# Kernel tuning notes

Hardware: AMD Instinct MI355X
Metric: run time of the kernel (lower is better)

## Reference

```python
import jax, jax.numpy as jnp
import numpy as np

N_NODES = 50000
N_EDGES = 1600000
D_IN = 128
D_HID = 128
D_OUT = 64
N_EXPERT = 16


def setup_inputs() -> dict:
    key = jax.random.key(0)
    ks = jax.random.split(key, 16)
    x = jax.random.normal(ks[0], (N_NODES, D_IN), dtype=jnp.float32)
    edge_index = jax.random.randint(ks[1], (2, N_EDGES), 0, N_NODES, dtype=jnp.int64)

    def lin(k, di, do):
        return jax.random.normal(k, (di, do), dtype=jnp.float32) / np.float32(np.sqrt(di))

    def expert_w(k, di, do):
        return jax.random.normal(k, (N_EXPERT, di, do), dtype=jnp.float32) / np.float32(np.sqrt(di))

    return {
        "x": x,
        "edge_index": edge_index,
        # layer 1 (MoE GCN conv: D_IN -> D_HID)
        "Wg1": lin(ks[2], D_IN, N_EXPERT), "bg1": jnp.zeros((N_EXPERT,), jnp.float32),
        "We1": expert_w(ks[3], D_IN, D_HID), "be1": jnp.zeros((N_EXPERT, D_HID), jnp.float32),
        "b1": jnp.zeros((D_HID,), jnp.float32),
        # layer 2 (MoE GCN conv: D_HID -> D_HID)
        "Wg2": lin(ks[4], D_HID, N_EXPERT), "bg2": jnp.zeros((N_EXPERT,), jnp.float32),
        "We2": expert_w(ks[5], D_HID, D_HID), "be2": jnp.zeros((N_EXPERT, D_HID), jnp.float32),
        "b2": jnp.zeros((D_HID,), jnp.float32),
        # layer 3 (plain GCNConv: D_HID -> D_OUT)
        "Wlast": lin(ks[6], D_HID, D_OUT), "blast": jnp.zeros((D_OUT,), jnp.float32),
    }


def _moe_linear(x, Wg, bg, We, be):
    # naive gate, top_k=1: route to argmax expert, combine weight 1.0
    scores = jax.nn.softmax(x @ Wg + bg, axis=-1)              # [N, E]
    idx = jnp.argmax(scores, axis=-1)                          # [N]
    y_all = jnp.einsum('nd,edh->neh', x, We) + be              # [N, E, H]
    onehot = jax.nn.one_hot(idx, We.shape[0], dtype=x.dtype)   # [N, E]
    y = jnp.einsum('neh,ne->nh', y_all, onehot)                # [N, H]
    return y, scores


def _scatter_add(h, edge_index, num_nodes):
    src, dst = edge_index[0], edge_index[1]
    return jax.ops.segment_sum(h[src], dst, num_segments=num_nodes)


def _moe_conv(x, edge_index, Wg, bg, We, be, bias):
    h, scores = _moe_linear(x, Wg, bg, We, be)
    out = _scatter_add(h, edge_index, x.shape[0]) + bias
    gate_std = jnp.mean(jnp.std(scores, axis=1, ddof=1))
    return out, gate_std


def reference(x, edge_index, Wg1, bg1, We1, be1, b1, Wg2, bg2, We2, be2, b2, Wlast, blast):
    # layer 1 + relu (dropout inactive in eval)
    h, g1 = _moe_conv(x, edge_index, Wg1, bg1, We1, be1, b1)
    h = jax.nn.relu(h)
    # layer 2 + relu
    h, g2 = _moe_conv(h, edge_index, Wg2, bg2, We2, be2, b2)
    h = jax.nn.relu(h)
    # final plain GCNConv (normalize=False, edge_weight=None)
    out = _scatter_add(h @ Wlast, edge_index, x.shape[0]) + blast
    gate_std_means = jnp.stack([g1, g2]).mean()
    gate_std_ngnn = jnp.asarray(1.0, dtype=x.dtype)
    return out, gate_std_means, gate_std_ngnn
```

## Files before the change

### kernel.cpp

```cpp
#include <hip/hip_runtime.h>
#include <math.h>

#define N_NODES 50000
#define N_EDGES 1600000
#define D_IN 128
#define D_HID 128
#define D_OUT 64
#define N_EXPERT 16
#define NB 8
#define GW 16
#define NYB 256
#define NBG 16
#define NGBLK (N_NODES / NBG)
#define XR4 33

#define NBUK 782
#define NFB 250
#define EPB (N_EDGES / NFB)
#define HM (NBUK * NFB)
#define NSB2 ((HM + 255) / 256)

__device__ __forceinline__ unsigned short f2bf(float f) {
    unsigned int u = __float_as_uint(f);
    return (unsigned short)((u + 0x7fffu + ((u >> 16) & 1u)) >> 16);
}
__device__ __forceinline__ float bf2f(unsigned short h) {
    return __uint_as_float((unsigned int)h << 16);
}

__global__ __launch_bounds__(256) void gate_kernel(
    const float* __restrict__ x, const float* __restrict__ Wg, const float* __restrict__ bg,
    int* __restrict__ eidx, float* __restrict__ gpart)
{
    __shared__ float xs[NBG][132];
    __shared__ float wgt[N_EXPERT][132];
    __shared__ float sred[NBG];
    const int n0 = blockIdx.x * NBG;
    const int t = threadIdx.x;

    {
        const float4* __restrict__ Wg4 = (const float4*)Wg;
        float4 v = Wg4[t];
        int d = t >> 2, e4 = (t & 3) * 4;
        wgt[e4 + 0][d] = v.x; wgt[e4 + 1][d] = v.y; wgt[e4 + 2][d] = v.z; wgt[e4 + 3][d] = v.w;
        v = Wg4[t + 256];
        d += 64;
        wgt[e4 + 0][d] = v.x; wgt[e4 + 1][d] = v.y; wgt[e4 + 2][d] = v.z; wgt[e4 + 3][d] = v.w;
    }
    {
        int id = t, row = id >> 5, c4 = id & 31;
        *(float4*)&xs[row][4 * c4] = ((const float4*)(x + (size_t)(n0 + row) * 128))[c4];
        id = t + 256; row = id >> 5; c4 = id & 31;
        *(float4*)&xs[row][4 * c4] = ((const float4*)(x + (size_t)(n0 + row) * 128))[c4];
    }
    __syncthreads();

    const int e = t & 15, j = t >> 4;
    float lg = bg[e];
    #pragma unroll
    for (int d4 = 0; d4 < 32; ++d4) {
        const float4 xv = *(const float4*)&xs[j][4 * d4];
        const float4 wv = *(const float4*)&wgt[e][4 * d4];
        lg = fmaf(xv.x, wv.x, lg);
        lg = fmaf(xv.y, wv.y, lg);
        lg = fmaf(xv.z, wv.z, lg);
        lg = fmaf(xv.w, wv.w, lg);
    }

    float mx = lg;
    #pragma unroll
    for (int m = 8; m >= 1; m >>= 1) mx = fmaxf(mx, __shfl_xor(mx, m, 16));
    const float ex = expf(lg - mx);
    float se = ex;
    #pragma unroll
    for (int m = 8; m >= 1; m >>= 1) se += __shfl_xor(se, m, 16);
    const float p = ex / se;
    const float dm = p - (1.f / 16.f);
    float var = dm * dm;
    #pragma unroll
    for (int m = 8; m >= 1; m >>= 1) var += __shfl_xor(var, m, 16);

    float bv = lg; int bi = e;
    #pragma unroll
    for (int m = 8; m >= 1; m >>= 1) {
        const float ov = __shfl_xor(bv, m, 16);
        const int oi = __shfl_xor(bi, m, 16);
        if (ov > bv || (ov == bv && oi < bi)) { bv = ov; bi = oi; }
    }
    if (e == 0) {
        eidx[n0 + j] = bi;
        sred[j] = sqrtf(var * (1.f / 15.f));
    }
    __syncthreads();
    if (t == 0) {
        float s = 0.f;
        #pragma unroll
        for (int jj = 0; jj < NBG; ++jj) s += sred[jj];
        gpart[blockIdx.x] = s;
    }
}

__global__ __launch_bounds__(256) void hist16_kernel(
    const int* __restrict__ eidx, int* __restrict__ ecnt)
{
    __shared__ int lcnt[N_EXPERT];
    const int t = threadIdx.x;
    const int n = blockIdx.x * 256 + t;
    if (t < N_EXPERT) lcnt[t] = 0;
    __syncthreads();
    if (n < N_NODES) atomicAdd(&lcnt[eidx[n]], 1);
    __syncthreads();
    if (t < N_EXPERT && lcnt[t] > 0) atomicAdd(&ecnt[t], lcnt[t]);
}

__global__ void scan16_kernel(const int* __restrict__ ecnt,
                              int* __restrict__ eoff, int* __restrict__ ecur)
{
    if (threadIdx.x == 0) {
        int s = 0;
        #pragma unroll
        for (int e = 0; e < N_EXPERT; ++e) { eoff[e] = s; ecur[e] = s; s += ecnt[e]; }
        eoff[N_EXPERT] = s;
    }
}

__global__ __launch_bounds__(256) void scatter16_kernel(
    const int* __restrict__ eidx, int* __restrict__ ecur, int* __restrict__ elist)
{
    __shared__ int lcnt[N_EXPERT];
    __shared__ int lbase[N_EXPERT];
    const int t = threadIdx.x;
    const int n = blockIdx.x * 256 + t;
    if (t < N_EXPERT) lcnt[t] = 0;
    __syncthreads();
    int e = 0, lpos = 0;
    if (n < N_NODES) { e = eidx[n]; lpos = atomicAdd(&lcnt[e], 1); }
    __syncthreads();
    if (t < N_EXPERT && lcnt[t] > 0) lbase[t] = atomicAdd(&ecur[t], lcnt[t]);
    __syncthreads();
    if (n < N_NODES) elist[lbase[e] + lpos] = n;
}

__global__ __launch_bounds__(64) void expert_gemm_kernel(
    const float* __restrict__ x, const float* __restrict__ We, const float* __restrict__ be,
    const int* __restrict__ eoff, const int* __restrict__ elist,
    unsigned short* __restrict__ y)
{
    __shared__ float xsd[GW * 132];
    const int e = blockIdx.x;
    const int t = threadIdx.x;
    const int row0 = eoff[e];
    const int row1 = eoff[e + 1];

    const float2* __restrict__ Wv2 = (const float2*)(We + (size_t)e * 16384);
    const float4* __restrict__ Xv = (const float4*)xsd;
    const float2 bv = ((const float2*)be)[e * 64 + t];

    for (int chunk = blockIdx.y;; chunk += (int)gridDim.y) {
        const int start = row0 + chunk * GW;
        if (start >= row1) break;

        #pragma unroll
        for (int i = 0; i < 8; ++i) {
            const int id = t + 64 * i;
            const int r = id >> 5;
            const int c4 = id & 31;
            const int idx = start + r;
            const int node = elist[idx < row1 ? idx : start];
            ((float4*)xsd)[r * XR4 + c4] = ((const float4*)(x + (size_t)node * 128))[c4];
        }
        __syncthreads();

        float2 acc[GW];
        #pragma unroll
        for (int k = 0; k < GW; ++k) acc[k] = bv;

        #pragma unroll 2
        for (int d4 = 0; d4 < 32; ++d4) {
            float2 w0 = Wv2[(4 * d4 + 0) * 64 + t];
            float2 w1 = Wv2[(4 * d4 + 1) * 64 + t];
            float2 w2 = Wv2[(4 * d4 + 2) * 64 + t];
            float2 w3 = Wv2[(4 * d4 + 3) * 64 + t];
            #pragma unroll
            for (int k = 0; k < GW; ++k) {
                const float4 xv = Xv[k * XR4 + d4];
                acc[k].x = fmaf(xv.x, w0.x, acc[k].x);
                acc[k].y = fmaf(xv.x, w0.y, acc[k].y);
                acc[k].x = fmaf(xv.y, w1.x, acc[k].x);
                acc[k].y = fmaf(xv.y, w1.y, acc[k].y);
                acc[k].x = fmaf(xv.z, w2.x, acc[k].x);
                acc[k].y = fmaf(xv.z, w2.y, acc[k].y);
                acc[k].x = fmaf(xv.w, w3.x, acc[k].x);
                acc[k].y = fmaf(xv.w, w3.y, acc[k].y);
            }
        }

        #pragma unroll
        for (int k = 0; k < GW; ++k) {
            const int idx = start + k;
            if (idx < row1) {
                ushort2 o;
                o.x = f2bf(acc[k].x);
                o.y = f2bf(acc[k].y);
                *(ushort2*)&y[(size_t)elist[idx] * 128 + 2 * t] = o;
            }
        }

        __syncthreads();
    }
}

__global__ __launch_bounds__(64) void last_kernel(
    const float* __restrict__ h, const float* __restrict__ W,
    unsigned short* __restrict__ y)
{
    __shared__ float xs[NB][128];
    const int n0 = blockIdx.x * NB, t = threadIdx.x;
    #pragma unroll
    for (int j = 0; j < NB; ++j) {
        xs[j][t] = h[(size_t)(n0 + j) * 128 + t];
        xs[j][t + 64] = h[(size_t)(n0 + j) * 128 + t + 64];
    }
    __syncthreads();
    float a0 = 0.f, a1 = 0.f, a2 = 0.f, a3 = 0.f;
    float a4 = 0.f, a5 = 0.f, a6 = 0.f, a7 = 0.f;
    #pragma unroll 4
    for (int d = 0; d < 128; ++d) {
        const float w = W[d * 64 + t];
        a0 = fmaf(xs[0][d], w, a0);
        a1 = fmaf(xs[1][d], w, a1);
        a2 = fmaf(xs[2][d], w, a2);
        a3 = fmaf(xs[3][d], w, a3);
        a4 = fmaf(xs[4][d], w, a4);
        a5 = fmaf(xs[5][d], w, a5);
        a6 = fmaf(xs[6][d], w, a6);
        a7 = fmaf(xs[7][d], w, a7);
    }
    y[(size_t)(n0 + 0) * 64 + t] = f2bf(a0);
    y[(size_t)(n0 + 1) * 64 + t] = f2bf(a1);
    y[(size_t)(n0 + 2) * 64 + t] = f2bf(a2);
    y[(size_t)(n0 + 3) * 64 + t] = f2bf(a3);
    y[(size_t)(n0 + 4) * 64 + t] = f2bf(a4);
    y[(size_t)(n0 + 5) * 64 + t] = f2bf(a5);
    y[(size_t)(n0 + 6) * 64 + t] = f2bf(a6);
    y[(size_t)(n0 + 7) * 64 + t] = f2bf(a7);
}

__global__ __launch_bounds__(256) void bhist_kernel(
    const int* __restrict__ edst, int* __restrict__ hist_g)
{
    __shared__ int lcnt[NBUK];
    const int t = threadIdx.x;
    const int b = blockIdx.x;
    for (int i = t; i < NBUK; i += 256) lcnt[i] = 0;
    __syncthreads();
    const int e0 = b * EPB;
    #pragma unroll 5
    for (int k = 0; k < EPB / 256; ++k)
        atomicAdd(&lcnt[edst[e0 + k * 256 + t] >> 6], 1);
    __syncthreads();
    for (int i = t; i < NBUK; i += 256) hist_g[i * NFB + b] = lcnt[i];
}

__global__ __launch_bounds__(256) void hpre_kernel(
    const int* __restrict__ hist_g, int* __restrict__ tsum)
{
    __shared__ int ws[4];
    const int t = threadIdx.x;
    const int idx = blockIdx.x * 256 + t;
    int v = (idx < HM) ? hist_g[idx] : 0;
    #pragma unroll
    for (int m = 32; m >= 1; m >>= 1) v += __shfl_xor(v, m, 64);
    if ((t & 63) == 0) ws[t >> 6] = v;
    __syncthreads();
    if (t == 0) tsum[blockIdx.x] = ws[0] + ws[1] + ws[2] + ws[3];
}

__global__ __launch_bounds__(1024) void hscan_kernel(
    const int* __restrict__ tsum, int* __restrict__ tbase, int* __restrict__ rowptr_last)
{
    __shared__ int buf[1024];
    const int t = threadIdx.x;
    const int v = (t < NSB2) ? tsum[t] : 0;
    buf[t] = v;
    __syncthreads();
    for (int off = 1; off < 1024; off <<= 1) {
        const int add = (t >= off) ? buf[t - off] : 0;
        __syncthreads();
        buf[t] += add;
        __syncthreads();
    }
    if (t < NSB2) tbase[t] = buf[t] - v;
    if (t == 0) rowptr_last[0] = N_EDGES;
}

__global__ __launch_bounds__(256) void hwb_kernel(
    const int* __restrict__ hist_g, const int* __restrict__ tbase,
    int* __restrict__ base_g)
{
    __shared__ int buf[256];
    const int t = threadIdx.x;
    const int idx = blockIdx.x * 256 + t;
    const int v = (idx < HM) ? hist_g[idx] : 0;
    buf[t] = v;
    __syncthreads();
    for (int off = 1; off < 256; off <<= 1) {
        const int add = (t >= off) ? buf[t - off] : 0;
        __syncthreads();
        buf[t] += add;
        __syncthreads();
    }
    if (idx < HM) base_g[idx] = buf[t] - v + tbase[blockIdx.x];
}

__global__ __launch_bounds__(256) void bscatter_kernel(
    const int* __restrict__ esrc, const int* __restrict__ edst,
    const int* __restrict__ base_g, unsigned int* __restrict__ packed)
{
    __shared__ int rcur[NBUK];
    const int t = threadIdx.x;
    const int b = blockIdx.x;
    for (int i = t; i < NBUK; i += 256) rcur[i] = base_g[i * NFB + b];
    __syncthreads();
    const int e0 = b * EPB;
    #pragma unroll 5
    for (int k = 0; k < EPB / 256; ++k) {
        const int i = e0 + k * 256 + t;
        const int src = esrc[i];
        const int dst = edst[i];
        const int p = atomicAdd(&rcur[dst >> 6], 1);
        packed[p] = ((unsigned int)dst << 16) | (unsigned int)src;
    }
}

__global__ __launch_bounds__(256) void bfine_kernel(
    const unsigned int* __restrict__ packed, const int* __restrict__ base_g,
    int* __restrict__ rowptr, unsigned short* __restrict__ csr_src)
{
    __shared__ int cnt64[64], cur64[64], sexcl[64];
    const int t = threadIdx.x;
    const int j = blockIdx.x;
    const int s0 = base_g[j * NFB];
    const int s1 = (j + 1 < NBUK) ? base_g[(j + 1) * NFB] : N_EDGES;
    if (t < 64) cnt64[t] = 0;
    __syncthreads();
    for (int i = s0 + t; i < s1; i += 256)
        atomicAdd(&cnt64[(packed[i] >> 16) & 63], 1);
    __syncthreads();
    if (t == 0) {
        int run = 0;
        #pragma unroll
        for (int l = 0; l < 64; ++l) { sexcl[l] = run; run += cnt64[l]; }
    }
    __syncthreads();
    if (t < 64) {
        cur64[t] = 0;
        const int n = (j << 6) + t;
        if (n < N_NODES) rowptr[n] = s0 + sexcl[t];
    }
    __syncthreads();
    for (int i = s0 + t; i < s1; i += 256) {
        const unsigned int pk = packed[i];
        const int dl = (pk >> 16) & 63;
        const int p = atomicAdd(&cur64[dl], 1);
        csr_src[s0 + sexcl[dl] + p] = (unsigned short)(pk & 0xffff);
    }
}

template <int D, bool RELU>
__global__ __launch_bounds__(D) void gather_kernel(
    const unsigned short* __restrict__ h, const int* __restrict__ rowptr,
    const unsigned short* __restrict__ csr_src, const float* __restrict__ bias,
    float* __restrict__ out)
{
    const int n = blockIdx.x, t = threadIdx.x;
    const int s0 = rowptr[n], s1 = rowptr[n + 1];
    float a0 = bias[t], a1 = 0.f, a2 = 0.f, a3 = 0.f;
    float a4 = 0.f, a5 = 0.f, a6 = 0.f, a7 = 0.f;
    int e = s0;
    for (; e + 7 < s1; e += 8) {
        const int i0 = csr_src[e + 0];
        const int i1 = csr_src[e + 1];
        const int i2 = csr_src[e + 2];
        const int i3 = csr_src[e + 3];
        const int i4 = csr_src[e + 4];
        const int i5 = csr_src[e + 5];
        const int i6 = csr_src[e + 6];
        const int i7 = csr_src[e + 7];
        a0 += bf2f(h[(size_t)i0 * D + t]);
        a1 += bf2f(h[(size_t)i1 * D + t]);
        a2 += bf2f(h[(size_t)i2 * D + t]);
        a3 += bf2f(h[(size_t)i3 * D + t]);
        a4 += bf2f(h[(size_t)i4 * D + t]);
        a5 += bf2f(h[(size_t)i5 * D + t]);
        a6 += bf2f(h[(size_t)i6 * D + t]);
        a7 += bf2f(h[(size_t)i7 * D + t]);
    }
    for (; e + 3 < s1; e += 4) {
        const int i0 = csr_src[e + 0];
        const int i1 = csr_src[e + 1];
        const int i2 = csr_src[e + 2];
        const int i3 = csr_src[e + 3];
        a0 += bf2f(h[(size_t)i0 * D + t]);
        a1 += bf2f(h[(size_t)i1 * D + t]);
        a2 += bf2f(h[(size_t)i2 * D + t]);
        a3 += bf2f(h[(size_t)i3 * D + t]);
    }
    for (; e < s1; ++e) a0 += bf2f(h[(size_t)csr_src[e] * D + t]);
    float acc = ((a0 + a1) + (a2 + a3)) + ((a4 + a5) + (a6 + a7));
    if (RELU) acc = fmaxf(acc, 0.f);
    out[(size_t)n * D + t] = acc;
}

__global__ __launch_bounds__(1024) void finalize_kernel(
    const float* __restrict__ gpart, float* __restrict__ out_tail)
{
    __shared__ float wsum[16];
    const int t = threadIdx.x;
    float s = 0.f;
    for (int i = t; i < 2 * NGBLK; i += 1024) s += gpart[i];
    #pragma unroll
    for (int m = 32; m >= 1; m >>= 1) s += __shfl_xor(s, m, 64);
    if ((t & 63) == 0) wsum[t >> 6] = s;
    __syncthreads();
    if (t == 0) {
        float tot = 0.f;
        #pragma unroll
        for (int w = 0; w < 16; ++w) tot += wsum[w];
        out_tail[0] = tot * (0.5f / (float)N_NODES);
        out_tail[1] = 1.0f;
    }
}

extern "C" void kernel_launch(void* const* d_in, const int* in_sizes, int n_in,
                              void* d_out, int out_size, void* d_ws, size_t ws_size,
                              hipStream_t stream)
{
    const float* x     = (const float*)d_in[0];
    const int*   edge  = (const int*)d_in[1];
    const float* Wg1   = (const float*)d_in[2];
    const float* bg1   = (const float*)d_in[3];
    const float* We1   = (const float*)d_in[4];
    const float* be1   = (const float*)d_in[5];
    const float* b1    = (const float*)d_in[6];
    const float* Wg2   = (const float*)d_in[7];
    const float* bg2   = (const float*)d_in[8];
    const float* We2   = (const float*)d_in[9];
    const float* be2   = (const float*)d_in[10];
    const float* b2    = (const float*)d_in[11];
    const float* Wlast = (const float*)d_in[12];
    const float* blast = (const float*)d_in[13];
    float* out = (float*)d_out;

    const int* esrc = edge;
    const int* edst = edge + N_EDGES;

    char* ws = (char*)d_ws;
    size_t off = 0;
    float* gpart = (float*)(ws + off); off += (size_t)2 * NGBLK * 4 + 252; off &= ~(size_t)255;
    float* A = (float*)(ws + off); off += (size_t)N_NODES * 128 * 4;
    float* B = (float*)(ws + off); off += (size_t)N_NODES * 128 * 4;
    int* rowptr = (int*)(ws + off); off += (size_t)(N_NODES + 1) * 4 + 252; off &= ~(size_t)255;
    int* eidx = (int*)(ws + off); off += (size_t)N_NODES * 4 + 252; off &= ~(size_t)255;
    unsigned short* csr_src = (unsigned short*)(ws + off); off += (size_t)N_EDGES * 2 + 252; off &= ~(size_t)255;
    int* elist = (int*)(ws + off); off += (size_t)N_NODES * 4 + 252; off &= ~(size_t)255;
    int* meta = (int*)(ws + off); off += 256;
    int* ecnt = meta;
    int* eoff = meta + 16;
    int* ecur = meta + 33;

    unsigned short* Abf = (unsigned short*)A;

    unsigned int* packed = (unsigned int*)A;
    int* hist_g = (int*)B;
    int* base_g = hist_g + HM;
    int* tsum   = base_g + HM;
    int* tbase  = tsum + NSB2;

    bhist_kernel<<<NFB, 256, 0, stream>>>(edst, hist_g);
    hpre_kernel<<<NSB2, 256, 0, stream>>>(hist_g, tsum);
    hscan_kernel<<<1, 1024, 0, stream>>>(tsum, tbase, rowptr + N_NODES);
    hwb_kernel<<<NSB2, 256, 0, stream>>>(hist_g, tbase, base_g);
    bscatter_kernel<<<NFB, 256, 0, stream>>>(esrc, edst, base_g, packed);
    bfine_kernel<<<NBUK, 256, 0, stream>>>(packed, base_g, rowptr, csr_src);

    const int nbk = (N_NODES + 255) / 256;

    gate_kernel<<<NGBLK, 256, 0, stream>>>(x, Wg1, bg1, eidx, gpart);
    hipMemsetAsync(ecnt, 0, 64, stream);
    hist16_kernel<<<nbk, 256, 0, stream>>>(eidx, ecnt);
    scan16_kernel<<<1, 64, 0, stream>>>(ecnt, eoff, ecur);
    scatter16_kernel<<<nbk, 256, 0, stream>>>(eidx, ecur, elist);
    expert_gemm_kernel<<<dim3(N_EXPERT, NYB), 64, 0, stream>>>(x, We1, be1, eoff, elist, Abf);
    gather_kernel<128, true><<<N_NODES, 128, 0, stream>>>(Abf, rowptr, csr_src, b1, B);

    gate_kernel<<<NGBLK, 256, 0, stream>>>(B, Wg2, bg2, eidx, gpart + NGBLK);
    hipMemsetAsync(ecnt, 0, 64, stream);
    hist16_kernel<<<nbk, 256, 0, stream>>>(eidx, ecnt);
    scan16_kernel<<<1, 64, 0, stream>>>(ecnt, eoff, ecur);
    scatter16_kernel<<<nbk, 256, 0, stream>>>(eidx, ecur, elist);
    expert_gemm_kernel<<<dim3(N_EXPERT, NYB), 64, 0, stream>>>(B, We2, be2, eoff, elist, Abf);
    gather_kernel<128, true><<<N_NODES, 128, 0, stream>>>(Abf, rowptr, csr_src, b2, B);

    last_kernel<<<N_NODES / NB, 64, 0, stream>>>(B, Wlast, Abf);
    gather_kernel<64, false><<<N_NODES, 64, 0, stream>>>(Abf, rowptr, csr_src, blast, out);

    finalize_kernel<<<1, 1024, 0, stream>>>(gpart, out + (size_t)N_NODES * 64);
}
```

Measured before the change: 420.1 us.

## Use persistent blocks with an atomic work queue for the expert GEMM

The expert GEMM previously ran on a fixed grid of 16 experts by 256 y-blocks, so experts holding more routed nodes looped over more chunks while other blocks sat idle. The scan kernel now also writes per-expert chunk offsets and resets a global counter. A fixed pool of 2048 blocks then claims chunks with an atomicAdd and finds each chunk's expert with a linear search. This is meant to balance work across imbalanced experts, at the cost of one atomic per chunk, an extra barrier per chunk, and reloading weight pointers whenever a block switches expert.

```diff
diff --git a/kernel.cpp b/kernel.cpp
--- a/kernel.cpp
+++ b/kernel.cpp
@@ -9,7 +9,7 @@
 #define N_EXPERT 16
 #define NB 8
 #define GW 16
-#define NYB 256
+#define NPB 2048
 #define NBG 16
 #define NGBLK (N_NODES / NBG)
 #define XR4 33
@@ -114,13 +114,20 @@
 }
 
 __global__ void scan16_kernel(const int* __restrict__ ecnt,
-                              int* __restrict__ eoff, int* __restrict__ ecur)
+                              int* __restrict__ eoff, int* __restrict__ ecur,
+                              int* __restrict__ coff, int* __restrict__ ctr)
 {
     if (threadIdx.x == 0) {
-        int s = 0;
-        #pragma unroll
-        for (int e = 0; e < N_EXPERT; ++e) { eoff[e] = s; ecur[e] = s; s += ecnt[e]; }
+        int s = 0, c = 0;
+        #pragma unroll
+        for (int e = 0; e < N_EXPERT; ++e) {
+            eoff[e] = s; ecur[e] = s; coff[e] = c;
+            s += ecnt[e];
+            c += (ecnt[e] + GW - 1) / GW;
+        }
         eoff[N_EXPERT] = s;
+        coff[N_EXPERT] = c;
+        ctr[0] = 0;
     }
 }
 
@@ -143,26 +150,34 @@
 
 __global__ __launch_bounds__(64) void expert_gemm_kernel(
     const float* __restrict__ x, const float* __restrict__ We, const float* __restrict__ be,
-    const int* __restrict__ eoff, const int* __restrict__ elist,
-    unsigned short* __restrict__ y)
+    const int* __restrict__ eoff, const int* __restrict__ coff,
+    const int* __restrict__ elist, unsigned short* __restrict__ y,
+    int* __restrict__ ctr)
 {
     __shared__ float xsd[GW * 132];
-    const int e = blockIdx.x;
-    const int t = threadIdx.x;
-    const int row0 = eoff[e];
-    const int row1 = eoff[e + 1];
-
-    const float2* __restrict__ Wv2 = (const float2*)(We + (size_t)e * 16384);
-    const float4* __restrict__ Xv = (const float4*)xsd;
-    const float2 bv = ((const float2*)be)[e * 64 + t];
-
-    for (int chunk = blockIdx.y;; chunk += (int)gridDim.y) {
-        const int start = row0 + chunk * GW;
-        if (start >= row1) break;
-
-        #pragma unroll
-        for (int i = 0; i < 8; ++i) {
-            const int id = t + 64 * i;
+    __shared__ int s_i;
+    const int t = threadIdx.x;
+    const int total = coff[N_EXPERT];
+
+    while (true) {
+        if (t == 0) s_i = atomicAdd(ctr, 1);
+        __syncthreads();
+        const int i = s_i;
+        if (i >= total) break;
+
+        int e = 0;
+        while (coff[e + 1] <= i) ++e;
+        const int row0 = eoff[e];
+        const int row1 = eoff[e + 1];
+        const int start = row0 + (i - coff[e]) * GW;
+
+        const float2* __restrict__ Wv2 = (const float2*)(We + (size_t)e * 16384);
+        const float4* __restrict__ Xv = (const float4*)xsd;
+        const float2 bv = ((const float2*)be)[e * 64 + t];
+
+        #pragma unroll
+        for (int s = 0; s < 8; ++s) {
+            const int id = t + 64 * s;
             const int r = id >> 5;
             const int c4 = id & 31;
             const int idx = start + r;
@@ -205,8 +220,6 @@
                 *(ushort2*)&y[(size_t)elist[idx] * 128 + 2 * t] = o;
             }
         }
-
-        __syncthreads();
     }
 }
 
@@ -464,10 +477,12 @@
     int* eidx = (int*)(ws + off); off += (size_t)N_NODES * 4 + 252; off &= ~(size_t)255;
     unsigned short* csr_src = (unsigned short*)(ws + off); off += (size_t)N_EDGES * 2 + 252; off &= ~(size_t)255;
     int* elist = (int*)(ws + off); off += (size_t)N_NODES * 4 + 252; off &= ~(size_t)255;
-    int* meta = (int*)(ws + off); off += 256;
+    int* meta = (int*)(ws + off); off += 512;
     int* ecnt = meta;
     int* eoff = meta + 16;
     int* ecur = meta + 33;
+    int* coff = meta + 49;
+    int* ctr  = meta + 66;
 
     unsigned short* Abf = (unsigned short*)A;
 
@@ -489,17 +504,17 @@
     gate_kernel<<<NGBLK, 256, 0, stream>>>(x, Wg1, bg1, eidx, gpart);
     hipMemsetAsync(ecnt, 0, 64, stream);
     hist16_kernel<<<nbk, 256, 0, stream>>>(eidx, ecnt);
-    scan16_kernel<<<1, 64, 0, stream>>>(ecnt, eoff, ecur);
+    scan16_kernel<<<1, 64, 0, stream>>>(ecnt, eoff, ecur, coff, ctr);
     scatter16_kernel<<<nbk, 256, 0, stream>>>(eidx, ecur, elist);
-    expert_gemm_kernel<<<dim3(N_EXPERT, NYB), 64, 0, stream>>>(x, We1, be1, eoff, elist, Abf);
+    expert_gemm_kernel<<<NPB, 64, 0, stream>>>(x, We1, be1, eoff, coff, elist, Abf, ctr);
     gather_kernel<128, true><<<N_NODES, 128, 0, stream>>>(Abf, rowptr, csr_src, b1, B);
 
     gate_kernel<<<NGBLK, 256, 0, stream>>>(B, Wg2, bg2, eidx, gpart + NGBLK);
     hipMemsetAsync(ecnt, 0, 64, stream);
     hist16_kernel<<<nbk, 256, 0, stream>>>(eidx, ecnt);
-    scan16_kernel<<<1, 64, 0, stream>>>(ecnt, eoff, ecur);
+    scan16_kernel<<<1, 64, 0, stream>>>(ecnt, eoff, ecur, coff, ctr);
     scatter16_kernel<<<nbk, 256, 0, stream>>>(eidx, ecur, elist);
-    expert_gemm_kernel<<<dim3(N_EXPERT, NYB), 64, 0, stream>>>(B, We2, be2, eoff, elist, Abf);
+    expert_gemm_kernel<<<NPB, 64, 0, stream>>>(B, We2, be2, eoff, coff, elist, Abf, ctr);
     gather_kernel<128, true><<<N_NODES, 128, 0, stream>>>(Abf, rowptr, csr_src, b2, B);
 
     last_kernel<<<N_NODES / NB, 64, 0, stream>>>(B, Wlast, Abf);
```

Result: slower. 435.7 us (+3.7%).
